# Kernel tuning notes

Hardware: AMD Instinct MI355X
Metric: run time of the kernel (lower is better)

The kernel has to match this reference:

```python
import jax, jax.numpy as jnp
import numpy as np


def _fake_quant(x, bits, axis):
    """AQT-style abs-max symmetric fake quantization.

    IntNumerics(bits, preserve_zero=True, preserve_max_val=True, clip=True,
    round=True) with AbsMaxCalibration: bound = 2^(bits-1)-1,
    scale = absmax/bound (stop-gradient), q = round(clip(x/scale)),
    dequant = q*scale. Round uses straight-through estimator.
    """
    bound = float(2 ** (bits - 1) - 1)
    absmax = jax.lax.stop_gradient(
        jnp.max(jnp.abs(x), axis=axis, keepdims=True))
    scale = absmax / bound
    scale = jnp.where(scale == 0.0, jnp.ones_like(scale), scale)
    s = x / scale
    clipped = jnp.clip(s, -bound, bound)  # clip_gradient=True semantics
    rounded = clipped + jax.lax.stop_gradient(jnp.round(clipped) - clipped)
    return rounded * scale


def setup_inputs() -> dict:
    key = jax.random.key(0)
    k1, k2, k3 = jax.random.split(key, 3)
    B, S, D, F = 4, 2048, 4096, 4096
    x = jax.random.normal(k1, (B, S, D), dtype=jnp.float32)
    # lecun_normal over (in, out)
    kernel = jax.random.normal(k2, (D, F), dtype=jnp.float32) / np.sqrt(D)
    bias = jax.random.normal(k3, (F,), dtype=jnp.float32) * 0.01
    return {"x": x, "kernel": kernel, "bias": bias}


def reference(x, kernel, bias):
    # int8 fake-quant of activations: abs-max over contracting (last) axis
    xq = _fake_quant(x, bits=8, axis=-1)
    # int8 fake-quant of kernel: abs-max over contracting axis (0) -> per out-col
    kq = _fake_quant(kernel, bits=8, axis=0)
    # quantized dot_general: contract last axis of x with axis 0 of kernel
    y = jnp.einsum('bsd,df->bsf', xq, kq)
    # int16 fake-quant of bias (calibration_axes=-1 over the whole vector)
    bq16 = _fake_quant(bias, bits=16, axis=-1)
    y = y + bq16[None, None, :]
    # int8 output requant, per-row abs-max over feature axis
    out = _fake_quant(y, bits=8, axis=-1)
    return out
```

## Files before the change

### kernel.cpp

```cpp
#include <hip/hip_runtime.h>
#include <stdint.h>

typedef int int32x4 __attribute__((ext_vector_type(4)));

#define M_ROWS 8192
#define K_DIM  4096
#define N_DIM  4096

#define GPTR(p) ((const __attribute__((address_space(1))) unsigned int*)(p))
#define LPTR(p) ((__attribute__((address_space(3))) unsigned int*)(p))

__device__ __forceinline__ float block_absmax_256(float v, float* red) {
#pragma unroll
  for (int off = 32; off > 0; off >>= 1)
    v = fmaxf(v, __shfl_down(v, off, 64));
  const int w = threadIdx.x >> 6;
  if ((threadIdx.x & 63) == 0) red[w] = v;
  __syncthreads();
  return fmaxf(fmaxf(red[0], red[1]), fmaxf(red[2], red[3]));
}

__global__ void quant_x_kernel(const float* __restrict__ x,
                               int8_t* __restrict__ qx,
                               float* __restrict__ sx) {
  __shared__ float red[4];
  const int row = blockIdx.x;
  const int t = threadIdx.x;
  const float4* xr = (const float4*)(x + (size_t)row * K_DIM);
  float4 v[4];
  float m = 0.0f;
#pragma unroll
  for (int i = 0; i < 4; ++i) {
    v[i] = xr[i * 256 + t];
    m = fmaxf(m, fmaxf(fmaxf(fabsf(v[i].x), fabsf(v[i].y)),
                       fmaxf(fabsf(v[i].z), fabsf(v[i].w))));
  }
  float amax = block_absmax_256(m, red);
  float scale = amax / 127.0f;
  if (scale == 0.0f) scale = 1.0f;
  if (t == 0) sx[row] = scale;
  int* qw = (int*)(qx + (size_t)row * K_DIM);
#pragma unroll
  for (int i = 0; i < 4; ++i) {
    float a = fminf(fmaxf(v[i].x / scale, -127.0f), 127.0f);
    float b = fminf(fmaxf(v[i].y / scale, -127.0f), 127.0f);
    float c = fminf(fmaxf(v[i].z / scale, -127.0f), 127.0f);
    float d = fminf(fmaxf(v[i].w / scale, -127.0f), 127.0f);
    int qa = (int)rintf(a), qb = (int)rintf(b), qc = (int)rintf(c), qd = (int)rintf(d);
    qw[i * 256 + t] =
        (qa & 255) | ((qb & 255) << 8) | ((qc & 255) << 16) | ((qd & 255) << 24);
  }
}

__global__ void colmax_kernel(const float* __restrict__ k,
                              float* __restrict__ cmp) {
  const int c = blockIdx.x * 256 + threadIdx.x;
  const int r0 = blockIdx.y * 128;
  float m = 0.0f;
  for (int i = 0; i < 128; ++i)
    m = fmaxf(m, fabsf(k[(size_t)(r0 + i) * N_DIM + c]));
  cmp[(size_t)blockIdx.y * N_DIM + c] = m;
}

__global__ void finalize_kernel(const float* __restrict__ cmp,
                                float* __restrict__ sk,
                                const float* __restrict__ bias,
                                float* __restrict__ bq) {
  __shared__ float red[4];
  const int t = threadIdx.x;
  if (blockIdx.x < 16) {
    const int c = blockIdx.x * 256 + t;
    float m = 0.0f;
#pragma unroll
    for (int i = 0; i < 32; ++i) m = fmaxf(m, cmp[(size_t)i * N_DIM + c]);
    float s = m / 127.0f;
    if (s == 0.0f) s = 1.0f;
    sk[c] = s;
  } else {
    float4 v[4];
    float m = 0.0f;
#pragma unroll
    for (int i = 0; i < 4; ++i) {
      v[i] = *(const float4*)(bias + t * 16 + i * 4);
      m = fmaxf(m, fmaxf(fmaxf(fabsf(v[i].x), fabsf(v[i].y)),
                         fmaxf(fabsf(v[i].z), fabsf(v[i].w))));
    }
    float amax = block_absmax_256(m, red);
    float s = amax / 32767.0f;
    if (s == 0.0f) s = 1.0f;
#pragma unroll
    for (int i = 0; i < 4; ++i) {
      float4 o;
      o.x = rintf(fminf(fmaxf(v[i].x / s, -32767.0f), 32767.0f)) * s;
      o.y = rintf(fminf(fmaxf(v[i].y / s, -32767.0f), 32767.0f)) * s;
      o.z = rintf(fminf(fmaxf(v[i].z / s, -32767.0f), 32767.0f)) * s;
      o.w = rintf(fminf(fmaxf(v[i].w / s, -32767.0f), 32767.0f)) * s;
      *(float4*)(bq + t * 16 + i * 4) = o;
    }
  }
}

__global__ void quant_kT_kernel(const float* __restrict__ kern,
                                const float* __restrict__ sk,
                                int8_t* __restrict__ qkT) {
  __shared__ int8_t tile[64][80];
  const int t = threadIdx.x;
  const int c0 = blockIdx.x * 64;
  const int r0 = blockIdx.y * 64;
  const int colg = (t & 15) * 4;
  const int row = t >> 4;
  float s[4];
#pragma unroll
  for (int j = 0; j < 4; ++j) s[j] = sk[c0 + colg + j];
#pragma unroll
  for (int i = 0; i < 4; ++i) {
    const int r = row + i * 16;
    float4 v = *(const float4*)&kern[(size_t)(r0 + r) * N_DIM + c0 + colg];
    tile[colg + 0][r] = (int8_t)rintf(fminf(fmaxf(v.x / s[0], -127.0f), 127.0f));
    tile[colg + 1][r] = (int8_t)rintf(fminf(fmaxf(v.y / s[1], -127.0f), 127.0f));
    tile[colg + 2][r] = (int8_t)rintf(fminf(fmaxf(v.z / s[2], -127.0f), 127.0f));
    tile[colg + 3][r] = (int8_t)rintf(fminf(fmaxf(v.w / s[3], -127.0f), 127.0f));
  }
  __syncthreads();
  const int f = t >> 2;
  const int seg = (t & 3) * 16;
  int4 w = *(const int4*)&tile[f][seg];
  *(int4*)(qkT + (size_t)(c0 + f) * K_DIM + r0 + seg) = w;
}

#define BM 256
#define BN 128
#define BK 64

__global__ __launch_bounds__(256, 2)
void gemm_kernel(const int8_t* __restrict__ qx,
                 const int8_t* __restrict__ qkT,
                 const float* __restrict__ sx,
                 const float* __restrict__ sk,
                 const float* __restrict__ bq,
                 float* __restrict__ out) {
  __shared__ int32x4 AsV[2048];
  char* As = (char*)AsV;

  const int t = threadIdx.x;
  const int w = t >> 6;
  const int l = t & 63;
  const int wm = w >> 1, wn = w & 1;
  const int rowBase = blockIdx.y * BM;
  const int colBase = blockIdx.x * BN;

  const int8_t* gA = qx + (size_t)(rowBase + (t >> 2)) * K_DIM
                        + (((t & 3) ^ ((t >> 2) & 3)) << 4);
  const int8_t* gB = qkT + (size_t)(colBase + wn * 64 + (l & 15)) * K_DIM
                         + ((l >> 4) << 4);

  int aoff[8];
#pragma unroll
  for (int mt = 0; mt < 8; ++mt)
    aoff[mt] = (wm * 128 + mt * 16 + (l & 15)) * 64 + (((l >> 4) ^ (l & 3)) << 4);

  int32x4 zero = {0, 0, 0, 0};
  int32x4 acc[8][4];
#pragma unroll
  for (int mt = 0; mt < 8; ++mt)
#pragma unroll
    for (int nt = 0; nt < 4; ++nt) acc[mt][nt] = zero;

  int32x4 bc[4], bn[4];

#pragma unroll
  for (int j = 0; j < 4; ++j)
    __builtin_amdgcn_global_load_lds(GPTR(gA + (size_t)j * 64 * K_DIM),
                                     LPTR(As + j * 4096 + w * 1024), 16, 0, 0);
#pragma unroll
  for (int nt = 0; nt < 4; ++nt)
    bc[nt] = *(const int32x4*)(gB + (size_t)nt * 16 * K_DIM);
  __syncthreads();

  int buf = 0;
  for (int i = 0; i < 63; ++i) {
    const int kn = (i + 1) * BK;
    char* dst = As + ((buf ^ 1) << 14) + w * 1024;
#pragma unroll
    for (int j = 0; j < 4; ++j)
      __builtin_amdgcn_global_load_lds(GPTR(gA + (size_t)j * 64 * K_DIM + kn),
                                       LPTR(dst + j * 4096), 16, 0, 0);
#pragma unroll
    for (int nt = 0; nt < 4; ++nt)
      bn[nt] = *(const int32x4*)(gB + (size_t)nt * 16 * K_DIM + kn);

    const char* Ab = As + (buf << 14);
    int32x4 af[8];
#pragma unroll
    for (int mt = 0; mt < 8; ++mt)
      af[mt] = *(const int32x4*)(Ab + aoff[mt]);
#pragma unroll
    for (int mt = 0; mt < 8; ++mt)
#pragma unroll
      for (int nt = 0; nt < 4; ++nt)
        acc[mt][nt] = __builtin_amdgcn_mfma_i32_16x16x64_i8(
            af[mt], bc[nt], acc[mt][nt], 0, 0, 0);

    __syncthreads();
#pragma unroll
    for (int nt = 0; nt < 4; ++nt) bc[nt] = bn[nt];
    buf ^= 1;
  }
  {
    const char* Ab = As + (buf << 14);
    int32x4 af[8];
#pragma unroll
    for (int mt = 0; mt < 8; ++mt)
      af[mt] = *(const int32x4*)(Ab + aoff[mt]);
#pragma unroll
    for (int mt = 0; mt < 8; ++mt)
#pragma unroll
      for (int nt = 0; nt < 4; ++nt)
        acc[mt][nt] = __builtin_amdgcn_mfma_i32_16x16x64_i8(
            af[mt], bc[nt], acc[mt][nt], 0, 0, 0);
  }

  const int lr = (l >> 4) * 4;
  const int lc = l & 15;
  float skc[4], bqc[4];
#pragma unroll
  for (int nt = 0; nt < 4; ++nt) {
    const int c = colBase + wn * 64 + nt * 16 + lc;
    skc[nt] = sk[c];
    bqc[nt] = bq[c];
  }
#pragma unroll
  for (int mt = 0; mt < 8; ++mt) {
    const int r0 = rowBase + wm * 128 + mt * 16 + lr;
    float sxr[4];
#pragma unroll
    for (int r = 0; r < 4; ++r) sxr[r] = sx[r0 + r];
#pragma unroll
    for (int nt = 0; nt < 4; ++nt) {
      const int c = colBase + wn * 64 + nt * 16 + lc;
#pragma unroll
      for (int r = 0; r < 4; ++r)
        out[(size_t)(r0 + r) * N_DIM + c] =
            (float)acc[mt][nt][r] * (sxr[r] * skc[nt]) + bqc[nt];
    }
  }
}

__global__ void requant_kernel(float* __restrict__ y) {
  __shared__ float red[4];
  const int row = blockIdx.x;
  const int t = threadIdx.x;
  float* yr = y + (size_t)row * N_DIM;
  float4 v[4];
  float m = 0.0f;
#pragma unroll
  for (int i = 0; i < 4; ++i) {
    v[i] = *(const float4*)(yr + i * 1024 + t * 4);
    m = fmaxf(m, fmaxf(fmaxf(fabsf(v[i].x), fabsf(v[i].y)),
                       fmaxf(fabsf(v[i].z), fabsf(v[i].w))));
  }
  float amax = block_absmax_256(m, red);
  float s = amax / 127.0f;
  if (s == 0.0f) s = 1.0f;
#pragma unroll
  for (int i = 0; i < 4; ++i) {
    float4 o;
    o.x = rintf(fminf(fmaxf(v[i].x / s, -127.0f), 127.0f)) * s;
    o.y = rintf(fminf(fmaxf(v[i].y / s, -127.0f), 127.0f)) * s;
    o.z = rintf(fminf(fmaxf(v[i].z / s, -127.0f), 127.0f)) * s;
    o.w = rintf(fminf(fmaxf(v[i].w / s, -127.0f), 127.0f)) * s;
    *(float4*)(yr + i * 1024 + t * 4) = o;
  }
}

extern "C" void kernel_launch(void* const* d_in, const int* in_sizes, int n_in,
                              void* d_out, int out_size, void* d_ws, size_t ws_size,
                              hipStream_t stream) {
  (void)in_sizes; (void)n_in; (void)out_size; (void)ws_size;
  const float* x    = (const float*)d_in[0];
  const float* kern = (const float*)d_in[1];
  const float* bias = (const float*)d_in[2];
  float* out = (float*)d_out;

  char* w8 = (char*)d_ws;
  int8_t* qx  = (int8_t*)w8;
  int8_t* qkT = (int8_t*)(w8 + 33554432);
  float* cmp  = (float*)(w8 + 33554432);
  float* sx   = (float*)(w8 + 50331648);
  float* sk   = (float*)(w8 + 50331648 + 32768);
  float* bq   = (float*)(w8 + 50331648 + 49152);

  quant_x_kernel<<<M_ROWS, 256, 0, stream>>>(x, qx, sx);
  colmax_kernel<<<dim3(16, 32), 256, 0, stream>>>(kern, cmp);
  finalize_kernel<<<17, 256, 0, stream>>>(cmp, sk, bias, bq);
  quant_kT_kernel<<<dim3(64, 64), 256, 0, stream>>>(kern, sk, qkT);
  gemm_kernel<<<dim3(N_DIM / BN, M_ROWS / BM), 256, 0, stream>>>(qx, qkT, sx, sk, bq, out);
  requant_kernel<<<M_ROWS, 256, 0, stream>>>(out);
}
```

Measured before the change: 519.6 us.

## Restructure int8 GEMM with 32x32x32 MFMA, LDS-staged B, BK=128 and block swizzle

```diff
diff --git a/kernel.cpp b/kernel.cpp
--- a/kernel.cpp
+++ b/kernel.cpp
@@ -1,7 +1,8 @@
 #include <hip/hip_runtime.h>
 #include <stdint.h>
 
-typedef int int32x4 __attribute__((ext_vector_type(4)));
+typedef int int32x4  __attribute__((ext_vector_type(4)));
+typedef int int32x16 __attribute__((ext_vector_type(16)));
 
 #define M_ROWS 8192
 #define K_DIM  4096
@@ -130,7 +131,7 @@
 
 #define BM 256
 #define BN 128
-#define BK 64
+#define BK 128
 
 __global__ __launch_bounds__(256, 2)
 void gemm_kernel(const int8_t* __restrict__ qx,
@@ -140,108 +141,98 @@
                  const float* __restrict__ bq,
                  float* __restrict__ out) {
   __shared__ int32x4 AsV[2048];
+  __shared__ int32x4 BsV[1024];
   char* As = (char*)AsV;
+  char* Bs = (char*)BsV;
 
   const int t = threadIdx.x;
   const int w = t >> 6;
   const int l = t & 63;
   const int wm = w >> 1, wn = w & 1;
-  const int rowBase = blockIdx.y * BM;
-  const int colBase = blockIdx.x * BN;
-
-  const int8_t* gA = qx + (size_t)(rowBase + (t >> 2)) * K_DIM
-                        + (((t & 3) ^ ((t >> 2) & 3)) << 4);
-  const int8_t* gB = qkT + (size_t)(colBase + wn * 64 + (l & 15)) * K_DIM
-                         + ((l >> 4) << 4);
-
-  int aoff[8];
-#pragma unroll
-  for (int mt = 0; mt < 8; ++mt)
-    aoff[mt] = (wm * 128 + mt * 16 + (l & 15)) * 64 + (((l >> 4) ^ (l & 3)) << 4);
-
-  int32x4 zero = {0, 0, 0, 0};
-  int32x4 acc[8][4];
-#pragma unroll
-  for (int mt = 0; mt < 8; ++mt)
-#pragma unroll
-    for (int nt = 0; nt < 4; ++nt) acc[mt][nt] = zero;
-
-  int32x4 bc[4], bn[4];
-
-#pragma unroll
-  for (int j = 0; j < 4; ++j)
-    __builtin_amdgcn_global_load_lds(GPTR(gA + (size_t)j * 64 * K_DIM),
-                                     LPTR(As + j * 4096 + w * 1024), 16, 0, 0);
-#pragma unroll
-  for (int nt = 0; nt < 4; ++nt)
-    bc[nt] = *(const int32x4*)(gB + (size_t)nt * 16 * K_DIM);
-  __syncthreads();
-
-  int buf = 0;
-  for (int i = 0; i < 63; ++i) {
-    const int kn = (i + 1) * BK;
-    char* dst = As + ((buf ^ 1) << 14) + w * 1024;
+
+  const int b = blockIdx.y * gridDim.x + blockIdx.x;
+  const int lb = (b & 7) * 128 + (b >> 3);
+  const int rowBase = (lb & 31) * BM;
+  const int colBase = (lb >> 5) * BN;
+
+  const int8_t* gA = qx  + (size_t)(rowBase + (t >> 3)) * K_DIM
+                         + (((t & 7) ^ ((t >> 3) & 7)) * 16);
+  const int8_t* gB = qkT + (size_t)(colBase + (t >> 3)) * K_DIM
+                         + (((t & 7) ^ ((t >> 3) & 7)) * 16);
+
+  int aoff[4], boff[2], soff[4];
+#pragma unroll
+  for (int mt = 0; mt < 4; ++mt)
+    aoff[mt] = (wm * 128 + mt * 32 + (l & 31)) * 128;
+#pragma unroll
+  for (int nt = 0; nt < 2; ++nt)
+    boff[nt] = (wn * 64 + nt * 32 + (l & 31)) * 128;
+#pragma unroll
+  for (int s = 0; s < 4; ++s)
+    soff[s] = ((s * 2 + (l >> 5)) ^ (l & 7)) * 16;
+
+  int32x16 acc[4][2];
+#pragma unroll
+  for (int mt = 0; mt < 4; ++mt)
+#pragma unroll
+    for (int nt = 0; nt < 2; ++nt)
+#pragma unroll
+      for (int r = 0; r < 16; ++r) acc[mt][nt][r] = 0;
+
+  for (int k0 = 0; k0 < K_DIM; k0 += BK) {
+    __syncthreads();
+#pragma unroll
+    for (int j = 0; j < 8; ++j)
+      __builtin_amdgcn_global_load_lds(
+          GPTR(gA + (size_t)j * 32 * K_DIM + k0),
+          LPTR(As + j * 4096 + w * 1024), 16, 0, 0);
 #pragma unroll
     for (int j = 0; j < 4; ++j)
-      __builtin_amdgcn_global_load_lds(GPTR(gA + (size_t)j * 64 * K_DIM + kn),
-                                       LPTR(dst + j * 4096), 16, 0, 0);
-#pragma unroll
-    for (int nt = 0; nt < 4; ++nt)
-      bn[nt] = *(const int32x4*)(gB + (size_t)nt * 16 * K_DIM + kn);
-
-    const char* Ab = As + (buf << 14);
-    int32x4 af[8];
-#pragma unroll
-    for (int mt = 0; mt < 8; ++mt)
-      af[mt] = *(const int32x4*)(Ab + aoff[mt]);
-#pragma unroll
-    for (int mt = 0; mt < 8; ++mt)
-#pragma unroll
-      for (int nt = 0; nt < 4; ++nt)
-        acc[mt][nt] = __builtin_amdgcn_mfma_i32_16x16x64_i8(
-            af[mt], bc[nt], acc[mt][nt], 0, 0, 0);
-
+      __builtin_amdgcn_global_load_lds(
+          GPTR(gB + (size_t)j * 32 * K_DIM + k0),
+          LPTR(Bs + j * 4096 + w * 1024), 16, 0, 0);
     __syncthreads();
-#pragma unroll
-    for (int nt = 0; nt < 4; ++nt) bc[nt] = bn[nt];
-    buf ^= 1;
-  }
-  {
-    const char* Ab = As + (buf << 14);
-    int32x4 af[8];
-#pragma unroll
-    for (int mt = 0; mt < 8; ++mt)
-      af[mt] = *(const int32x4*)(Ab + aoff[mt]);
-#pragma unroll
-    for (int mt = 0; mt < 8; ++mt)
-#pragma unroll
-      for (int nt = 0; nt < 4; ++nt)
-        acc[mt][nt] = __builtin_amdgcn_mfma_i32_16x16x64_i8(
-            af[mt], bc[nt], acc[mt][nt], 0, 0, 0);
-  }
-
-  const int lr = (l >> 4) * 4;
-  const int lc = l & 15;
-  float skc[4], bqc[4];
-#pragma unroll
-  for (int nt = 0; nt < 4; ++nt) {
-    const int c = colBase + wn * 64 + nt * 16 + lc;
-    skc[nt] = sk[c];
-    bqc[nt] = bq[c];
-  }
-#pragma unroll
-  for (int mt = 0; mt < 8; ++mt) {
-    const int r0 = rowBase + wm * 128 + mt * 16 + lr;
-    float sxr[4];
-#pragma unroll
-    for (int r = 0; r < 4; ++r) sxr[r] = sx[r0 + r];
-#pragma unroll
-    for (int nt = 0; nt < 4; ++nt) {
-      const int c = colBase + wn * 64 + nt * 16 + lc;
-#pragma unroll
-      for (int r = 0; r < 4; ++r)
-        out[(size_t)(r0 + r) * N_DIM + c] =
-            (float)acc[mt][nt][r] * (sxr[r] * skc[nt]) + bqc[nt];
+
+#pragma unroll
+    for (int s = 0; s < 4; ++s) {
+      int32x4 af[4], bf[2];
+#pragma unroll
+      for (int mt = 0; mt < 4; ++mt)
+        af[mt] = *(const int32x4*)(As + aoff[mt] + soff[s]);
+#pragma unroll
+      for (int nt = 0; nt < 2; ++nt)
+        bf[nt] = *(const int32x4*)(Bs + boff[nt] + soff[s]);
+#pragma unroll
+      for (int mt = 0; mt < 4; ++mt)
+#pragma unroll
+        for (int nt = 0; nt < 2; ++nt)
+          acc[mt][nt] = __builtin_amdgcn_mfma_i32_32x32x32_i8(
+              af[mt], bf[nt], acc[mt][nt], 0, 0, 0);
+    }
+  }
+
+  float skc[2], bqc[2];
+  int cc[2];
+#pragma unroll
+  for (int nt = 0; nt < 2; ++nt) {
+    cc[nt] = colBase + wn * 64 + nt * 32 + (l & 31);
+    skc[nt] = sk[cc[nt]];
+    bqc[nt] = bq[cc[nt]];
+  }
+#pragma unroll
+  for (int mt = 0; mt < 4; ++mt) {
+    const int rbase = rowBase + wm * 128 + mt * 32 + (l >> 5) * 4;
+#pragma unroll
+    for (int g = 0; g < 4; ++g) {
+#pragma unroll
+      for (int q = 0; q < 4; ++q) {
+        const int r = rbase + q + 8 * g;
+        const float sxv = sx[r];
+#pragma unroll
+        for (int nt = 0; nt < 2; ++nt)
+          out[(size_t)r * N_DIM + cc[nt]] =
+              (float)acc[mt][nt][g * 4 + q] * (sxv * skc[nt]) + bqc[nt];
+      }
     }
   }
 }
@@ -294,6 +285,6 @@
   colmax_kernel<<<dim3(16, 32), 256, 0, stream>>>(kern, cmp);
   finalize_kernel<<<17, 256, 0, stream>>>(cmp, sk, bias, bq);
   quant_kT_kernel<<<dim3(64, 64), 256, 0, stream>>>(kern, sk, qkT);
-  gemm_kernel<<<dim3(N_DIM / BN, M_ROWS / BM), 256, 0, stream>>>(qx, qkT, sx, sk, bq, out);
+  gemm_kernel<<<dim3(32, 32), 256, 0, stream>>>(qx, qkT, sx, sk, bq, out);
   requant_kernel<<<M_ROWS, 256, 0, stream>>>(out);
 }
```

Result: faster. 485.0 us (-6.7%).
